# Kernel optimization log

Hardware: AMD Instinct MI355X
Metric: run time of the kernel (lower is better)

Reference implementation:

```python
import jax, jax.numpy as jnp
import numpy as np

PROJ_EPS = 1e-5   # hyperbolic_projection keeps ||x|| <= 1 - PROJ_EPS
MIN_NORM = 1e-15  # numerical floor for norms/denominators
N, D, E, L = 100000, 128, 800000, 2


def _norm(x):
    return jnp.linalg.norm(x, axis=-1, keepdims=True)


def hyperbolic_projection(x):
    n = _norm(x)
    max_n = 1.0 - PROJ_EPS
    scale = jnp.where(n > max_n, max_n / jnp.maximum(n, MIN_NORM), 1.0)
    return x * scale


def exp_map_zero(v):
    n = jnp.maximum(_norm(v), MIN_NORM)
    return jnp.tanh(n) * v / n


def log_map_zero(y):
    n = jnp.maximum(_norm(y), MIN_NORM)
    nc = jnp.clip(n, MIN_NORM, 1.0 - PROJ_EPS)
    return jnp.arctanh(nc) * y / n


def mobius_addition(u, v):
    uu = jnp.sum(u * u, -1, keepdims=True)
    vv = jnp.sum(v * v, -1, keepdims=True)
    uv = jnp.sum(u * v, -1, keepdims=True)
    num = (1.0 + 2.0 * uv + vv) * u + (1.0 - uu) * v
    den = 1.0 + 2.0 * uv + uu * vv
    return num / jnp.maximum(den, MIN_NORM)


def setup_inputs() -> dict:
    key = jax.random.key(0)
    k = jax.random.split(key, 5)
    ent = jax.random.normal(k[0], (N, D), jnp.float32) * 0.1
    W = jax.random.normal(k[1], (L, D, D), jnp.float32) * (1.0 / np.sqrt(D))
    bias = jnp.zeros((L, D), jnp.float32)
    rows = jax.random.randint(k[2], (E,), 0, N)
    cols = jax.random.randint(k[3], (E,), 0, N)
    vals = jax.random.uniform(k[4], (E,), jnp.float32) / 8.0  # ~row-normalized adj values
    return {"ent_embeddings": ent, "W": W, "bias": bias,
            "adj_rows": rows, "adj_cols": cols, "adj_vals": vals}


def _gcn_layer(x, W_l, b_l, rows, cols, vals, use_act):
    # log map to tangent at origin, linear transform
    t = log_map_zero(x)                      # [N, D]
    m = t @ W_l                              # [N, D]
    # sparse adjacency matmul: adj @ m  (COO gather-scale-scatter)
    msg = m[cols] * vals[:, None]            # [E, D]
    agg = jax.ops.segment_sum(msg, rows, num_segments=N)  # [N, D]
    h = hyperbolic_projection(exp_map_zero(agg))
    # hyperbolic bias via mobius addition
    bh = hyperbolic_projection(exp_map_zero(b_l[None, :]))  # [1, D]
    h = hyperbolic_projection(mobius_addition(h, bh))
    if use_act:
        h = hyperbolic_projection(exp_map_zero(jnp.tanh(log_map_zero(h))))
    return h


def reference(ent_embeddings, W, bias, adj_rows, adj_cols, adj_vals):
    x = hyperbolic_projection(ent_embeddings)
    for l in range(L):
        use_act = (l < L - 1)  # tanh on all but last layer
        h = _gcn_layer(x, W[l], bias[l], adj_rows, adj_cols, adj_vals, use_act)
        # mobius residual connection with previous layer output
        x = hyperbolic_projection(mobius_addition(h, x))
    return x
```

## Files before the change

kernel.cpp:

```cpp
#include <hip/hip_runtime.h>
#include <math.h>

#define D 128
#define PROJ_EPS 1e-5f
#define MAX_NN (1.0f - PROJ_EPS)
#define MIN_NORM 1e-15f
#define ROWS_PER_BLOCK 2048

struct __align__(8) Edge { int c; float v; };

typedef __attribute__((ext_vector_type(8))) short bf16x8;
typedef __attribute__((ext_vector_type(4))) float f32x4;

__device__ inline unsigned short f2bf(float f) {
    unsigned u = __float_as_uint(f);
    unsigned r = (u + 0x7FFFu + ((u >> 16) & 1u)) >> 16;
    return (unsigned short)r;
}
__device__ inline float bf2f(unsigned short h) {
    return __uint_as_float(((unsigned)h) << 16);
}

__device__ inline float wave_sum(float v) {
#pragma unroll
    for (int off = 32; off; off >>= 1) v += __shfl_xor(v, off, 64);
    return v;
}
__device__ inline float g16sum(float v) {
#pragma unroll
    for (int off = 8; off; off >>= 1) v += __shfl_xor(v, off, 64);
    return v;
}
__device__ inline void g16sum2(float& a, float& b) {
#pragma unroll
    for (int off = 8; off; off >>= 1) {
        a += __shfl_xor(a, off, 64);
        b += __shfl_xor(b, off, 64);
    }
}
__device__ inline float frcp(float x) { return __builtin_amdgcn_rcpf(x); }
__device__ inline float fsqrt_(float x) { return __builtin_amdgcn_sqrtf(x); }
__device__ inline float tanh_pos(float x) {
    float e = __expf(-2.f * x);
    return (1.f - e) * frcp(1.f + e);
}
__device__ inline float tanh_sgn(float x) {
    float ax = fabsf(x);
    float e = __expf(-2.f * ax);
    float r = (1.f - e) * frcp(1.f + e);
    return copysignf(r, x);
}
__device__ inline float atanh_clip(float x) {
    return 0.5f * __logf((1.f + x) * frcp(1.f - x));
}

__device__ inline float2 mk2(float a, float b) { float2 r; r.x = a; r.y = b; return r; }
__device__ inline float2 bc2(float a) { return mk2(a, a); }
__device__ inline float2 pk_fma2(float2 a, float2 b, float2 c) {
    float2 d;
    asm("v_pk_fma_f32 %0, %1, %2, %3" : "=v"(d) : "v"(a), "v"(b), "v"(c));
    return d;
}
__device__ inline float2 pk_mul2(float2 a, float2 b) {
    float2 d;
    asm("v_pk_mul_f32 %0, %1, %2" : "=v"(d) : "v"(a), "v"(b));
    return d;
}
__device__ inline float2 up2(unsigned u) {
    uint2 t; t.x = u << 16; t.y = u & 0xffff0000u;
    float2 r; r.x = __uint_as_float(t.x); r.y = __uint_as_float(t.y);
    return r;
}

__global__ void hist_kernel(const int* __restrict__ rows, int* __restrict__ counts, int e) {
    int i = blockIdx.x * blockDim.x + threadIdx.x;
    if (i < e) atomicAdd(&counts[rows[i]], 1);
}

__global__ __launch_bounds__(256) void partial_kernel(const int* __restrict__ counts,
                                                      int* __restrict__ partials, int n) {
    int t = threadIdx.x;
    int start = blockIdx.x * ROWS_PER_BLOCK + t * 8;
    int s = 0;
#pragma unroll
    for (int j = 0; j < 8; ++j) {
        int i = start + j;
        if (i < n) s += counts[i];
    }
    int lane = t & 63, wv = t >> 6;
#pragma unroll
    for (int o = 32; o; o >>= 1) s += __shfl_xor(s, o, 64);
    __shared__ int wsum[4];
    if (lane == 0) wsum[wv] = s;
    __syncthreads();
    if (t == 0) partials[blockIdx.x] = wsum[0] + wsum[1] + wsum[2] + wsum[3];
}

__global__ void scan_partials(int* __restrict__ partials, int npart) {
    __shared__ int buf[1024];
    int t = threadIdx.x;
    int v = (t < npart) ? partials[t] : 0;
    buf[t] = v;
    __syncthreads();
    for (int o = 1; o < 1024; o <<= 1) {
        int x = (t >= o) ? buf[t - o] : 0;
        __syncthreads();
        buf[t] += x;
        __syncthreads();
    }
    if (t < npart) partials[t] = buf[t] - v;
}

__global__ __launch_bounds__(256) void rowptr_kernel(const int* __restrict__ counts,
                                                     const int* __restrict__ partials,
                                                     int* __restrict__ row_ptr,
                                                     int* __restrict__ cursor, int n, int e) {
    int t = threadIdx.x;
    int start = blockIdx.x * ROWS_PER_BLOCK + t * 8;
    int c[8];
    int s = 0;
#pragma unroll
    for (int j = 0; j < 8; ++j) {
        int i = start + j;
        c[j] = (i < n) ? counts[i] : 0;
        s += c[j];
    }
    int lane = t & 63, wv = t >> 6;
    int inc = s;
#pragma unroll
    for (int o = 1; o < 64; o <<= 1) {
        int tt = __shfl_up(inc, o, 64);
        if (lane >= o) inc += tt;
    }
    __shared__ int wsum[4];
    if (lane == 63) wsum[wv] = inc;
    __syncthreads();
    if (t == 0) {
        int acc = 0;
        for (int w = 0; w < 4; ++w) { int tmp = wsum[w]; wsum[w] = acc; acc += tmp; }
    }
    __syncthreads();
    int run = partials[blockIdx.x] + wsum[wv] + (inc - s);
#pragma unroll
    for (int j = 0; j < 8; ++j) {
        int i = start + j;
        if (i < n) {
            row_ptr[i] = run;
            cursor[i] = run;
            run += c[j];
        }
    }
    if (blockIdx.x == 0 && t == 0) row_ptr[n] = e;
}

__global__ void scatter_kernel(const int* __restrict__ rows, const int* __restrict__ cols,
                               const float* __restrict__ vals, int* __restrict__ cursor,
                               Edge* __restrict__ eds, int e) {
    int i = blockIdx.x * blockDim.x + threadIdx.x;
    if (i < e) {
        int r = rows[i];
        int pos = atomicAdd(&cursor[r], 1);
        Edge ed; ed.c = cols[i]; ed.v = vals[i];
        eds[pos] = ed;
    }
}

__global__ __launch_bounds__(256) void proj_init(const float* __restrict__ ent,
                                                 float* __restrict__ x,
                                                 float* __restrict__ logscale,
                                                 float* __restrict__ xnorm2, int n) {
    int wid = (int)((blockIdx.x * (size_t)blockDim.x + threadIdx.x) >> 6);
    int lane = threadIdx.x & 63;
    if (wid >= n) return;
    float2 v = *(const float2*)(ent + (size_t)wid * D + 2 * lane);
    float nrm = sqrtf(wave_sum(v.x * v.x + v.y * v.y));
    float scale = (nrm > MAX_NN) ? MAX_NN / fmaxf(nrm, MIN_NORM) : 1.0f;
    float px = v.x * scale, py = v.y * scale;
    float n2 = fmaxf(sqrtf(wave_sum(px * px + py * py)), MIN_NORM);
    float nc = fminf(fmaxf(n2, MIN_NORM), MAX_NN);
    float ls = atanhf(nc) / n2;
    *(float2*)(x + (size_t)wid * D + 2 * lane) = make_float2(px, py);
    if (lane == 0) { logscale[wid] = ls; xnorm2[wid] = n2 * n2; }
}

__global__ void bias_prep(const float* __restrict__ bias, float* __restrict__ bh,
                          float* __restrict__ vvb) {
    int l = blockIdx.x;
    int lane = threadIdx.x;
    float2 b2 = *(const float2*)(bias + (size_t)l * D + 2 * lane);
    float nn = fmaxf(sqrtf(wave_sum(b2.x * b2.x + b2.y * b2.y)), MIN_NORM);
    float s = tanhf(nn) / nn;
    float bx = b2.x * s, by = b2.y * s;
    float pn = sqrtf(wave_sum(bx * bx + by * by));
    float sc = (pn > MAX_NN) ? MAX_NN / fmaxf(pn, MIN_NORM) : 1.0f;
    bx *= sc; by *= sc;
    float vv = wave_sum(bx * bx + by * by);
    *(float2*)(bh + (size_t)l * D + 2 * lane) = make_float2(bx, by);
    if (lane == 0) vvb[l] = vv;
}

__global__ __launch_bounds__(256, 3) void logmap_gemm(const float* __restrict__ x,
                                                      const float* __restrict__ logscale,
                                                      const float* __restrict__ W,
                                                      unsigned short* __restrict__ m, int n,
                                                      int ntiles) {
    __shared__ char lds[16384];
    const int t = threadIdx.x;
    const int wid = t >> 6, lane = t & 63;
    const int lcol = lane & 15, lkg = lane >> 4;
    const int colbase = wid * 32;

    bf16x8 Bh[4][2], Bl[4][2];
#pragma unroll
    for (int ki = 0; ki < 4; ++ki) {
#pragma unroll
        for (int cf = 0; cf < 2; ++cf) {
            const float* wp = W + (size_t)(ki * 32 + lkg * 8) * D + colbase + cf * 16 + lcol;
#pragma unroll
            for (int e = 0; e < 8; ++e) {
                float f = wp[(size_t)e * D];
                unsigned short h = f2bf(f);
                Bh[ki][cf][e] = (short)h;
                Bl[ki][cf][e] = (short)f2bf(f - bf2f(h));
            }
        }
    }

    for (int tile = blockIdx.x; tile < ntiles; tile += gridDim.x) {
        const int row0 = tile * 32;
        __syncthreads();
#pragma unroll
        for (int p = t; p < 512; p += 256) {
            int fi = p >> 6, ln = p & 63;
            int rf = fi >> 2, ki = fi & 3;
            int row = row0 + rf * 16 + (ln & 15);
            int k0 = ki * 32 + (ln >> 4) * 8;
            float v[8];
            if (row < n) {
                float ls = logscale[row];
                const float* xp = x + (size_t)row * D + k0;
                *(float4*)&v[0] = *(const float4*)xp;
                *(float4*)&v[4] = *(const float4*)(xp + 4);
#pragma unroll
                for (int e = 0; e < 8; ++e) v[e] *= ls;
            } else {
#pragma unroll
                for (int e = 0; e < 8; ++e) v[e] = 0.f;
            }
            bf16x8 hi, lo;
#pragma unroll
            for (int e = 0; e < 8; ++e) {
                unsigned short h = f2bf(v[e]);
                hi[e] = (short)h;
                lo[e] = (short)f2bf(v[e] - bf2f(h));
            }
            *(bf16x8*)(lds + fi * 1024 + ln * 16) = hi;
            *(bf16x8*)(lds + 8192 + fi * 1024 + ln * 16) = lo;
        }
        __syncthreads();

        f32x4 acc[2][2];
#pragma unroll
        for (int rf = 0; rf < 2; ++rf)
#pragma unroll
            for (int cf = 0; cf < 2; ++cf) acc[rf][cf] = (f32x4){0.f, 0.f, 0.f, 0.f};

#pragma unroll
        for (int ki = 0; ki < 4; ++ki) {
            bf16x8 Ah[2], Al[2];
#pragma unroll
            for (int rf = 0; rf < 2; ++rf) {
                Ah[rf] = *(const bf16x8*)(lds + (rf * 4 + ki) * 1024 + lane * 16);
                Al[rf] = *(const bf16x8*)(lds + 8192 + (rf * 4 + ki) * 1024 + lane * 16);
            }
#pragma unroll
            for (int rf = 0; rf < 2; ++rf)
#pragma unroll
                for (int cf = 0; cf < 2; ++cf) {
                    acc[rf][cf] = __builtin_amdgcn_mfma_f32_16x16x32_bf16(Ah[rf], Bh[ki][cf], acc[rf][cf], 0, 0, 0);
                    acc[rf][cf] = __builtin_amdgcn_mfma_f32_16x16x32_bf16(Ah[rf], Bl[ki][cf], acc[rf][cf], 0, 0, 0);
                    acc[rf][cf] = __builtin_amdgcn_mfma_f32_16x16x32_bf16(Al[rf], Bh[ki][cf], acc[rf][cf], 0, 0, 0);
                }
        }

#pragma unroll
        for (int rf = 0; rf < 2; ++rf)
#pragma unroll
            for (int cf = 0; cf < 2; ++cf)
#pragma unroll
                for (int r = 0; r < 4; ++r) {
                    int row = row0 + rf * 16 + lkg * 4 + r;
                    if (row < n)
                        m[(size_t)row * D + colbase + cf * 16 + lcol] = f2bf(acc[rf][cf][r]);
                }
    }
}

__global__ __launch_bounds__(256) void aggregate(const unsigned short* __restrict__ m,
                                                 const int* __restrict__ row_ptr,
                                                 const Edge* __restrict__ eds,
                                                 const float* __restrict__ bh,
                                                 const float* __restrict__ vvb_p,
                                                 float* __restrict__ x,
                                                 float* __restrict__ logscale,
                                                 float* __restrict__ xnorm2,
                                                 int n, int use_act, int last) {
    int wv = (int)((blockIdx.x * (size_t)blockDim.x + threadIdx.x) >> 6);
    int lane = threadIdx.x & 63;
    int q = lane >> 4, li = lane & 15;
    if (wv * 4 >= n) return;
    int r = wv * 4 + q;
    bool active = (r < n);

    int beg = 0, end = 0;
    if (active) { beg = row_ptr[r]; end = row_ptr[r + 1]; }

    const char* mB = (const char*)m + ((size_t)li << 4);
    float2 A01 = bc2(0.f), A23 = bc2(0.f), A45 = bc2(0.f), A67 = bc2(0.f);
    int e = beg;
    for (; e + 4 <= end; e += 4) {
#pragma unroll
        for (int j = 0; j < 4; ++j) {
            Edge ee = eds[e + j];
            uint4 g = *(const uint4*)(mB + ((size_t)(unsigned)ee.c << 8));
            float2 v = bc2(ee.v);
            A01 = pk_fma2(up2(g.x), v, A01); A23 = pk_fma2(up2(g.y), v, A23);
            A45 = pk_fma2(up2(g.z), v, A45); A67 = pk_fma2(up2(g.w), v, A67);
        }
    }
    for (; e < end; ++e) {
        Edge ee = eds[e];
        uint4 g = *(const uint4*)(mB + ((size_t)(unsigned)ee.c << 8));
        float2 v = bc2(ee.v);
        A01 = pk_fma2(up2(g.x), v, A01); A23 = pk_fma2(up2(g.y), v, A23);
        A45 = pk_fma2(up2(g.z), v, A45); A67 = pk_fma2(up2(g.w), v, A67);
    }

    float4 bv0 = *(const float4*)(bh + 8 * li);
    float4 bv1 = *(const float4*)(bh + 8 * li + 4);
    float2 b01 = mk2(bv0.x, bv0.y), b23 = mk2(bv0.z, bv0.w);
    float2 b45 = mk2(bv1.x, bv1.y), b67 = mk2(bv1.z, bv1.w);
    float vvb = *vvb_p;

    float2 daa = pk_fma2(A67, A67, pk_fma2(A45, A45, pk_fma2(A23, A23, pk_mul2(A01, A01))));
    float2 dab = pk_fma2(A67, b67, pk_fma2(A45, b45, pk_fma2(A23, b23, pk_mul2(A01, b01))));
    float saa = daa.x + daa.y, sab = dab.x + dab.y;
    g16sum2(saa, sab);

    float na = fmaxf(fsqrt_(saa), MIN_NORM);
    float th = tanh_pos(na);
    float s1 = th * frcp(na);
    float nh = th;
    if (th > MAX_NN) { s1 *= MAX_NN * frcp(th); nh = MAX_NN; }
    float2 vs1 = bc2(s1);
    float2 H01 = pk_mul2(A01, vs1), H23 = pk_mul2(A23, vs1);
    float2 H45 = pk_mul2(A45, vs1), H67 = pk_mul2(A67, vs1);
    float uu = nh * nh;
    float uv = s1 * sab;

    float ca = 1.f + 2.f * uv + vvb;
    float cb = 1.f - uu;
    float den = fmaxf(1.f + 2.f * uv + uu * vvb, MIN_NORM);
    float nsq = fmaxf(ca * ca * uu + 2.f * ca * cb * uv + cb * cb * vvb, 0.f);
    float rden = frcp(den);
    float n2 = fsqrt_(nsq) * rden;
    float s2 = rden;
    if (n2 > MAX_NN) { s2 *= MAX_NN * frcp(n2); n2 = MAX_NN; }
    float2 vca = bc2(ca), vcb = bc2(cb), vs2 = bc2(s2);
    float2 P01 = pk_mul2(pk_fma2(H01, vca, pk_mul2(b01, vcb)), vs2);
    float2 P23 = pk_mul2(pk_fma2(H23, vca, pk_mul2(b23, vcb)), vs2);
    float2 P45 = pk_mul2(pk_fma2(H45, vca, pk_mul2(b45, vcb)), vs2);
    float2 P67 = pk_mul2(pk_fma2(H67, vca, pk_mul2(b67, vcb)), vs2);

    float4 xa = active ? *(const float4*)(x + (size_t)r * D + 8 * li)
                       : make_float4(0.f, 0.f, 0.f, 0.f);
    float4 xb = active ? *(const float4*)(x + (size_t)r * D + 8 * li + 4)
                       : make_float4(0.f, 0.f, 0.f, 0.f);
    float2 xo01 = mk2(xa.x, xa.y), xo23 = mk2(xa.z, xa.w);
    float2 xo45 = mk2(xb.x, xb.y), xo67 = mk2(xb.z, xb.w);

    float2 Q01, Q23, Q45, Q67;
    float uu3, uv3;
    if (use_act) {
        float nnv = fmaxf(n2, MIN_NORM);
        float nc = fminf(fmaxf(n2, MIN_NORM), MAX_NN);
        float ls2 = atanh_clip(nc) * frcp(nnv);
        float2 vls = bc2(ls2);
        float2 Z01 = pk_mul2(P01, vls), Z23 = pk_mul2(P23, vls);
        float2 Z45 = pk_mul2(P45, vls), Z67 = pk_mul2(P67, vls);
        float2 T01 = mk2(tanh_sgn(Z01.x), tanh_sgn(Z01.y));
        float2 T23 = mk2(tanh_sgn(Z23.x), tanh_sgn(Z23.y));
        float2 T45 = mk2(tanh_sgn(Z45.x), tanh_sgn(Z45.y));
        float2 T67 = mk2(tanh_sgn(Z67.x), tanh_sgn(Z67.y));
        float2 dtt = pk_fma2(T67, T67, pk_fma2(T45, T45, pk_fma2(T23, T23, pk_mul2(T01, T01))));
        float2 dtx = pk_fma2(T67, xo67, pk_fma2(T45, xo45, pk_fma2(T23, xo23, pk_mul2(T01, xo01))));
        float stt = dtt.x + dtt.y, stx = dtx.x + dtx.y;
        g16sum2(stt, stx);
        float n3 = fmaxf(fsqrt_(stt), MIN_NORM);
        float th3 = tanh_pos(n3);
        float s3 = th3 * frcp(n3);
        float nh3 = th3;
        if (th3 > MAX_NN) { s3 *= MAX_NN * frcp(th3); nh3 = MAX_NN; }
        float2 vs3 = bc2(s3);
        Q01 = pk_mul2(T01, vs3); Q23 = pk_mul2(T23, vs3);
        Q45 = pk_mul2(T45, vs3); Q67 = pk_mul2(T67, vs3);
        uu3 = nh3 * nh3;
        uv3 = s3 * stx;
    } else {
        float2 dpx = pk_fma2(P67, xo67, pk_fma2(P45, xo45, pk_fma2(P23, xo23, pk_mul2(P01, xo01))));
        float suv = g16sum(dpx.x + dpx.y);
        Q01 = P01; Q23 = P23; Q45 = P45; Q67 = P67;
        uu3 = n2 * n2;
        uv3 = suv;
    }

    float vv = active ? xnorm2[r] : 0.f;
    ca = 1.f + 2.f * uv3 + vv;
    cb = 1.f - uu3;
    den = fmaxf(1.f + 2.f * uv3 + uu3 * vv, MIN_NORM);
    nsq = fmaxf(ca * ca * uu3 + 2.f * ca * cb * uv3 + cb * cb * vv, 0.f);
    rden = frcp(den);
    float n4 = fsqrt_(nsq) * rden;
    float s4 = rden;
    if (n4 > MAX_NN) { s4 *= MAX_NN * frcp(n4); n4 = MAX_NN; }
    float2 vca2 = bc2(ca), vcb2 = bc2(cb), vs4 = bc2(s4);
    float2 O01 = pk_mul2(pk_fma2(Q01, vca2, pk_mul2(xo01, vcb2)), vs4);
    float2 O23 = pk_mul2(pk_fma2(Q23, vca2, pk_mul2(xo23, vcb2)), vs4);
    float2 O45 = pk_mul2(pk_fma2(Q45, vca2, pk_mul2(xo45, vcb2)), vs4);
    float2 O67 = pk_mul2(pk_fma2(Q67, vca2, pk_mul2(xo67, vcb2)), vs4);

    if (active) {
        *(float4*)(x + (size_t)r * D + 8 * li) = make_float4(O01.x, O01.y, O23.x, O23.y);
        *(float4*)(x + (size_t)r * D + 8 * li + 4) = make_float4(O45.x, O45.y, O67.x, O67.y);
        if (li == 0) {
            xnorm2[r] = n4 * n4;
            if (!last) {
                float nnv = fmaxf(n4, MIN_NORM);
                float nc = fminf(fmaxf(n4, MIN_NORM), MAX_NN);
                logscale[r] = atanh_clip(nc) * frcp(nnv);
            }
        }
    }
}

extern "C" void kernel_launch(void* const* d_in, const int* in_sizes, int n_in,
                              void* d_out, int out_size, void* d_ws, size_t ws_size,
                              hipStream_t stream) {
    const float* ent  = (const float*)d_in[0];
    const float* W    = (const float*)d_in[1];
    const float* bias = (const float*)d_in[2];
    const int* rows   = (const int*)d_in[3];
    const int* cols   = (const int*)d_in[4];
    const float* vals = (const float*)d_in[5];
    float* x = (float*)d_out;

    const int n = in_sizes[0] / D;
    const int e = in_sizes[3];
    const int nlayers = in_sizes[1] / (D * D);
    const int npart = (n + ROWS_PER_BLOCK - 1) / ROWS_PER_BLOCK;
    const int ntiles = (n + 31) / 32;

    char* ws = (char*)d_ws;
    size_t off = 0;
    auto alloc = [&](size_t bytes) {
        void* p = ws + off;
        off += (bytes + 255) & ~(size_t)255;
        return p;
    };
    unsigned short* m = (unsigned short*)alloc((size_t)n * D * sizeof(unsigned short));
    float* logscale = (float*)alloc((size_t)n * sizeof(float));
    float* xnorm2   = (float*)alloc((size_t)n * sizeof(float));
    int*   counts   = (int*)alloc((size_t)n * sizeof(int));
    int*   row_ptr  = (int*)alloc((size_t)(n + 1) * sizeof(int));
    int*   cursor   = (int*)alloc((size_t)n * sizeof(int));
    int*   partials = (int*)alloc((size_t)(npart > 1024 ? npart : 1024) * sizeof(int));
    float* bhb      = (float*)alloc((size_t)nlayers * D * sizeof(float));
    float* vvb      = (float*)alloc((size_t)nlayers * sizeof(float));
    Edge*  eds      = (Edge*)alloc((size_t)e * sizeof(Edge));

    hipMemsetAsync(counts, 0, (size_t)n * sizeof(int), stream);
    hist_kernel<<<(e + 255) / 256, 256, 0, stream>>>(rows, counts, e);
    partial_kernel<<<npart, 256, 0, stream>>>(counts, partials, n);
    scan_partials<<<1, 1024, 0, stream>>>(partials, npart);
    rowptr_kernel<<<npart, 256, 0, stream>>>(counts, partials, row_ptr, cursor, n, e);
    scatter_kernel<<<(e + 255) / 256, 256, 0, stream>>>(rows, cols, vals, cursor, eds, e);

    bias_prep<<<nlayers, 64, 0, stream>>>(bias, bhb, vvb);
    proj_init<<<(n + 3) / 4, 256, 0, stream>>>(ent, x, logscale, xnorm2, n);

    for (int l = 0; l < nlayers; ++l) {
        logmap_gemm<<<782, 256, 0, stream>>>(x, logscale, W + (size_t)l * D * D, m, n, ntiles);
        int use_act = (l < nlayers - 1) ? 1 : 0;
        aggregate<<<(n + 15) / 16, 256, 0, stream>>>(m, row_ptr, eds, bhb + (size_t)l * D,
                                                     vvb + l, x, logscale, xnorm2, n,
                                                     use_act, (l == nlayers - 1) ? 1 : 0);
    }
}
```

Before: 280.4 us.

## Pad CSR rows to multiples of four and use hardware packed bf16 conversion

```diff
diff --git a/kernel.cpp b/kernel.cpp
--- a/kernel.cpp
+++ b/kernel.cpp
@@ -12,13 +12,10 @@
 typedef __attribute__((ext_vector_type(8))) short bf16x8;
 typedef __attribute__((ext_vector_type(4))) float f32x4;
 
-__device__ inline unsigned short f2bf(float f) {
-    unsigned u = __float_as_uint(f);
-    unsigned r = (u + 0x7FFFu + ((u >> 16) & 1u)) >> 16;
-    return (unsigned short)r;
-}
-__device__ inline float bf2f(unsigned short h) {
-    return __uint_as_float(((unsigned)h) << 16);
+__device__ inline unsigned cvt_pk_bf16(float a, float b) {
+    unsigned r;
+    asm("v_cvt_pk_bf16_f32 %0, %1, %2" : "=v"(r) : "v"(a), "v"(b));
+    return r;
 }
 
 __device__ inline float wave_sum(float v) {
@@ -85,7 +82,7 @@
 #pragma unroll
     for (int j = 0; j < 8; ++j) {
         int i = start + j;
-        if (i < n) s += counts[i];
+        if (i < n) s += (counts[i] + 3) & ~3;
     }
     int lane = t & 63, wv = t >> 6;
 #pragma unroll
@@ -114,7 +111,7 @@
 __global__ __launch_bounds__(256) void rowptr_kernel(const int* __restrict__ counts,
                                                      const int* __restrict__ partials,
                                                      int* __restrict__ row_ptr,
-                                                     int* __restrict__ cursor, int n, int e) {
+                                                     int* __restrict__ cursor, int n) {
     int t = threadIdx.x;
     int start = blockIdx.x * ROWS_PER_BLOCK + t * 8;
     int c[8];
@@ -122,7 +119,7 @@
 #pragma unroll
     for (int j = 0; j < 8; ++j) {
         int i = start + j;
-        c[j] = (i < n) ? counts[i] : 0;
+        c[j] = (i < n) ? ((counts[i] + 3) & ~3) : 0;
         s += c[j];
     }
     int lane = t & 63, wv = t >> 6;
@@ -148,9 +145,9 @@
             row_ptr[i] = run;
             cursor[i] = run;
             run += c[j];
-        }
-    }
-    if (blockIdx.x == 0 && t == 0) row_ptr[n] = e;
+            if (i == n - 1) row_ptr[n] = run;
+        }
+    }
 }
 
 __global__ void scatter_kernel(const int* __restrict__ rows, const int* __restrict__ cols,
@@ -216,13 +213,23 @@
 #pragma unroll
         for (int cf = 0; cf < 2; ++cf) {
             const float* wp = W + (size_t)(ki * 32 + lkg * 8) * D + colbase + cf * 16 + lcol;
-#pragma unroll
-            for (int e = 0; e < 8; ++e) {
-                float f = wp[(size_t)e * D];
-                unsigned short h = f2bf(f);
-                Bh[ki][cf][e] = (short)h;
-                Bl[ki][cf][e] = (short)f2bf(f - bf2f(h));
+            float f[8];
+#pragma unroll
+            for (int e2 = 0; e2 < 8; ++e2) f[e2] = wp[(size_t)e2 * D];
+            unsigned hw[4], lw[4];
+#pragma unroll
+            for (int p = 0; p < 4; ++p) {
+                float a = f[2 * p], b = f[2 * p + 1];
+                unsigned h = cvt_pk_bf16(a, b);
+                float ha = __uint_as_float(h << 16);
+                float hb = __uint_as_float(h & 0xffff0000u);
+                hw[p] = h;
+                lw[p] = cvt_pk_bf16(a - ha, b - hb);
             }
+            uint4 uh = make_uint4(hw[0], hw[1], hw[2], hw[3]);
+            uint4 ul = make_uint4(lw[0], lw[1], lw[2], lw[3]);
+            Bh[ki][cf] = *(bf16x8*)&uh;
+            Bl[ki][cf] = *(bf16x8*)&ul;
         }
     }
 
@@ -242,20 +249,23 @@
                 *(float4*)&v[0] = *(const float4*)xp;
                 *(float4*)&v[4] = *(const float4*)(xp + 4);
 #pragma unroll
-                for (int e = 0; e < 8; ++e) v[e] *= ls;
+                for (int e2 = 0; e2 < 8; ++e2) v[e2] *= ls;
             } else {
 #pragma unroll
-                for (int e = 0; e < 8; ++e) v[e] = 0.f;
+                for (int e2 = 0; e2 < 8; ++e2) v[e2] = 0.f;
             }
-            bf16x8 hi, lo;
-#pragma unroll
-            for (int e = 0; e < 8; ++e) {
-                unsigned short h = f2bf(v[e]);
-                hi[e] = (short)h;
-                lo[e] = (short)f2bf(v[e] - bf2f(h));
+            unsigned hv[4], lv[4];
+#pragma unroll
+            for (int pp = 0; pp < 4; ++pp) {
+                float a = v[2 * pp], b = v[2 * pp + 1];
+                unsigned h = cvt_pk_bf16(a, b);
+                float ha = __uint_as_float(h << 16);
+                float hb = __uint_as_float(h & 0xffff0000u);
+                hv[pp] = h;
+                lv[pp] = cvt_pk_bf16(a - ha, b - hb);
             }
-            *(bf16x8*)(lds + fi * 1024 + ln * 16) = hi;
-            *(bf16x8*)(lds + 8192 + fi * 1024 + ln * 16) = lo;
+            *(uint4*)(lds + fi * 1024 + ln * 16) = make_uint4(hv[0], hv[1], hv[2], hv[3]);
+            *(uint4*)(lds + 8192 + fi * 1024 + ln * 16) = make_uint4(lv[0], lv[1], lv[2], lv[3]);
         }
         __syncthreads();
 
@@ -288,10 +298,12 @@
 #pragma unroll
             for (int cf = 0; cf < 2; ++cf)
 #pragma unroll
-                for (int r = 0; r < 4; ++r) {
-                    int row = row0 + rf * 16 + lkg * 4 + r;
-                    if (row < n)
-                        m[(size_t)row * D + colbase + cf * 16 + lcol] = f2bf(acc[rf][cf][r]);
+                for (int pr = 0; pr < 2; ++pr) {
+                    unsigned u = cvt_pk_bf16(acc[rf][cf][2 * pr], acc[rf][cf][2 * pr + 1]);
+                    int row = row0 + rf * 16 + lkg * 4 + 2 * pr;
+                    int col = colbase + cf * 16 + lcol;
+                    if (row < n) m[(size_t)row * D + col] = (unsigned short)u;
+                    if (row + 1 < n) m[(size_t)(row + 1) * D + col] = (unsigned short)(u >> 16);
                 }
     }
 }
@@ -315,10 +327,26 @@
     int beg = 0, end = 0;
     if (active) { beg = row_ptr[r]; end = row_ptr[r + 1]; }
 
+    float vv = active ? xnorm2[r] : 0.f;
+    float4 xa = active ? *(const float4*)(x + (size_t)r * D + 8 * li)
+                       : make_float4(0.f, 0.f, 0.f, 0.f);
+    float4 xb = active ? *(const float4*)(x + (size_t)r * D + 8 * li + 4)
+                       : make_float4(0.f, 0.f, 0.f, 0.f);
+
     const char* mB = (const char*)m + ((size_t)li << 4);
     float2 A01 = bc2(0.f), A23 = bc2(0.f), A45 = bc2(0.f), A67 = bc2(0.f);
     int e = beg;
-    for (; e + 4 <= end; e += 4) {
+    for (; e + 8 <= end; e += 8) {
+#pragma unroll
+        for (int j = 0; j < 8; ++j) {
+            Edge ee = eds[e + j];
+            uint4 g = *(const uint4*)(mB + ((size_t)(unsigned)ee.c << 8));
+            float2 v = bc2(ee.v);
+            A01 = pk_fma2(up2(g.x), v, A01); A23 = pk_fma2(up2(g.y), v, A23);
+            A45 = pk_fma2(up2(g.z), v, A45); A67 = pk_fma2(up2(g.w), v, A67);
+        }
+    }
+    if (e < end) {
 #pragma unroll
         for (int j = 0; j < 4; ++j) {
             Edge ee = eds[e + j];
@@ -327,13 +355,6 @@
             A01 = pk_fma2(up2(g.x), v, A01); A23 = pk_fma2(up2(g.y), v, A23);
             A45 = pk_fma2(up2(g.z), v, A45); A67 = pk_fma2(up2(g.w), v, A67);
         }
-    }
-    for (; e < end; ++e) {
-        Edge ee = eds[e];
-        uint4 g = *(const uint4*)(mB + ((size_t)(unsigned)ee.c << 8));
-        float2 v = bc2(ee.v);
-        A01 = pk_fma2(up2(g.x), v, A01); A23 = pk_fma2(up2(g.y), v, A23);
-        A45 = pk_fma2(up2(g.z), v, A45); A67 = pk_fma2(up2(g.w), v, A67);
     }
 
     float4 bv0 = *(const float4*)(bh + 8 * li);
@@ -372,10 +393,6 @@
     float2 P45 = pk_mul2(pk_fma2(H45, vca, pk_mul2(b45, vcb)), vs2);
     float2 P67 = pk_mul2(pk_fma2(H67, vca, pk_mul2(b67, vcb)), vs2);
 
-    float4 xa = active ? *(const float4*)(x + (size_t)r * D + 8 * li)
-                       : make_float4(0.f, 0.f, 0.f, 0.f);
-    float4 xb = active ? *(const float4*)(x + (size_t)r * D + 8 * li + 4)
-                       : make_float4(0.f, 0.f, 0.f, 0.f);
     float2 xo01 = mk2(xa.x, xa.y), xo23 = mk2(xa.z, xa.w);
     float2 xo45 = mk2(xb.x, xb.y), xo67 = mk2(xb.z, xb.w);
 
@@ -414,7 +431,6 @@
         uv3 = suv;
     }
 
-    float vv = active ? xnorm2[r] : 0.f;
     ca = 1.f + 2.f * uv3 + vv;
     cb = 1.f - uu3;
     den = fmaxf(1.f + 2.f * uv3 + uu3 * vv, MIN_NORM);
@@ -459,6 +475,7 @@
     const int nlayers = in_sizes[1] / (D * D);
     const int npart = (n + ROWS_PER_BLOCK - 1) / ROWS_PER_BLOCK;
     const int ntiles = (n + 31) / 32;
+    const size_t e_cap = (size_t)e + 3u * (size_t)n;
 
     char* ws = (char*)d_ws;
     size_t off = 0;
@@ -476,13 +493,14 @@
     int*   partials = (int*)alloc((size_t)(npart > 1024 ? npart : 1024) * sizeof(int));
     float* bhb      = (float*)alloc((size_t)nlayers * D * sizeof(float));
     float* vvb      = (float*)alloc((size_t)nlayers * sizeof(float));
-    Edge*  eds      = (Edge*)alloc((size_t)e * sizeof(Edge));
+    Edge*  eds      = (Edge*)alloc(e_cap * sizeof(Edge));
 
     hipMemsetAsync(counts, 0, (size_t)n * sizeof(int), stream);
+    hipMemsetAsync(eds, 0, e_cap * sizeof(Edge), stream);
     hist_kernel<<<(e + 255) / 256, 256, 0, stream>>>(rows, counts, e);
     partial_kernel<<<npart, 256, 0, stream>>>(counts, partials, n);
     scan_partials<<<1, 1024, 0, stream>>>(partials, npart);
-    rowptr_kernel<<<npart, 256, 0, stream>>>(counts, partials, row_ptr, cursor, n, e);
+    rowptr_kernel<<<npart, 256, 0, stream>>>(counts, partials, row_ptr, cursor, n);
     scatter_kernel<<<(e + 255) / 256, 256, 0, stream>>>(rows, cols, vals, cursor, eds, e);
 
     bias_prep<<<nlayers, 64, 0, stream>>>(bias, bhb, vvb);
```

After: 273.0 us (median of 2 runs). -2.7%, faster.
